# Kernel optimization log

Measured on AMD Instinct MI355X. Metric: run time of the kernel, lower is better.

Reference implementation:

```python
import jax, jax.numpy as jnp
import numpy as np
import math

INF = 1e12  # constant.INFINITY_NUMBER in the original repo


def setup_inputs() -> dict:
    key = jax.random.key(0)
    ks = jax.random.split(key, 12)
    B, S, W, D = 16, 512, 8, 768
    M, Wm = 2, 64
    U, Wu = 32, 16
    V = 32000
    words = jax.random.randint(ks[0], (B, S, W), 0, V)
    masks = jax.random.randint(ks[1], (B, S, W), 0, 2).astype(bool)
    main = jax.random.randint(ks[2], (B, M, Wm), 0, V)
    main_mask = jax.random.randint(ks[3], (B, M, Wm), 0, 2).astype(bool)
    user = jax.random.randint(ks[4], (B, U, Wu), 0, V)
    user_mask = jax.random.randint(ks[5], (B, U, Wu), 0, 2).astype(bool)
    # sparse-ish dependency adjacency
    adj = (jax.random.uniform(ks[6], (B, S, S)) < 0.05).astype(jnp.float32)
    emb_weight = jax.random.normal(ks[7], (V, D), jnp.float32) * 0.02
    K_w = jax.random.normal(ks[8], (D, D), jnp.float32) * (1.0 / math.sqrt(D))
    K_b = jnp.zeros((D,), jnp.float32)
    Q_w = jax.random.normal(ks[9], (D, D), jnp.float32) * (1.0 / math.sqrt(D))
    Q_b = jnp.zeros((D,), jnp.float32)
    return {"words": words, "masks": masks, "main": main, "main_mask": main_mask,
            "user": user, "user_mask": user_mask, "adj": adj,
            "emb_weight": emb_weight, "K_w": K_w, "K_b": K_b, "Q_w": Q_w, "Q_b": Q_b}


def _masked_max(embs, mask, axis):
    # masked_fill(mask, -INF) -> max(axis) ; caller fixes residual -INF rows
    return jnp.max(jnp.where(mask[..., None], -INF, embs), axis=axis)


def reference(words, masks, main, main_mask, user, user_mask, adj,
              emb_weight, K_w, K_b, Q_w, Q_b):
    D = emb_weight.shape[1]

    word_embs = emb_weight[words]   # [B,S,W,D]
    main_embs = emb_weight[main]    # [B,M,Wm,D]
    user_embs = emb_weight[user]    # [B,U,Wu,D]

    # node mask from adjacency: True where node has no in/out edges
    mask = ((adj.sum(axis=2) + adj.sum(axis=1)) == 0)[:, :, None]  # [B,S,1]

    # main: masked max-pool over word pieces, zero fully-masked rows
    main_e = _masked_max(main_embs, main_mask, axis=2)             # [B,M,D]
    main_e = jnp.where(main_e == -INF, 0.0, main_e)

    # user: masked max-pool over word pieces then over users
    user_e = _masked_max(user_embs, user_mask, axis=2)             # [B,U,D]
    user_e = jnp.max(user_e, axis=1)                               # [B,D]
    user_e = jnp.where(user_e == -INF, 0.0, user_e)

    # token embeddings: masked max-pool over word pieces (no -INF fix in original)
    g = _masked_max(word_embs, masks, axis=2)                      # [B,S,D]

    # single-head attention: softmax(K g (Q g)^T / sqrt(D)) @ g
    key_ = g @ K_w.T + K_b                                         # [B,S,D]
    query = g @ Q_w.T + Q_b                                        # [B,S,D]
    scores = jnp.einsum('bsd,btd->bst', key_, query) / math.sqrt(D)
    dense_graph = jax.nn.softmax(scores, axis=2)                   # [B,S,S]
    gcn_out = jnp.einsum('bst,btd->bsd', dense_graph, g)           # [B,S,D]

    adj_sm = jax.nn.softmax(adj, axis=2)

    return (gcn_out, mask, dense_graph, adj_sm,
            jnp.squeeze(main_e), jnp.squeeze(user_e))
```

## Files before the change

kernel.cpp:

```cpp
#include <hip/hip_runtime.h>
#include <hip/hip_bf16.h>
#include <math.h>

static constexpr int Bn = 16, Sn = 512, Wn = 8, Dn = 768;
static constexpr int Mn_ = 2, WMn = 64;
static constexpr int Un = 32, WUn = 16;

#define INF_VAL 1e12f
#define INV_SQRT_D 0.03608439182435161f

static constexpr size_t OFF_GCN   = 0;
static constexpr size_t OFF_MASK  = 6291456;
static constexpr size_t OFF_DENSE = 6299648;
static constexpr size_t OFF_ADJ   = 10493952;
static constexpr size_t OFF_MAIN  = 14688256;
static constexpr size_t OFF_USER  = 14712832;

static constexpr size_t WSB_GBF     = 0;
static constexpr size_t WSB_GT      = 12582912;
static constexpr size_t WSB_DENSEBF = 25165824;
static constexpr size_t WSB_HBF     = 33554432;
static constexpr size_t WSB_KWT     = 46137344;
static constexpr size_t WSB_QWT     = 47316992;
static constexpr size_t WSB_MT      = 48496640;
static constexpr size_t WSB_PARTU   = 49676288;
static constexpr size_t WSB_PARTM   = 51249152;
static constexpr size_t WSB_KBAR    = 51642368;
static constexpr size_t WSB_QBAR    = 51648512;
static constexpr size_t WSB_U       = 51654656;
static constexpr size_t WSB_V       = 51660800;
static constexpr size_t WSB_VA      = 51666944;
static constexpr size_t WSB_VB      = 51673088;
static constexpr size_t WSB_CONSTS  = 51679232;
static constexpr size_t WSB_QS      = 51679296;
static constexpr size_t WSB_KQ      = 51712064;
static constexpr size_t WSB_GA      = 51744832;
static constexpr size_t WSB_GB      = 51777600;
static constexpr size_t WSB_COLSUM  = 51810368;
static constexpr size_t WSB_FLAGS   = 51843136;
static constexpr size_t WSB_ROWSUM  = 51875904;
static constexpr size_t WSB_UVU     = 51908672;
static constexpr size_t WSB_UVV     = 51957824;
static constexpr size_t WSB_UVA     = 52006976;
static constexpr size_t WSB_UVB     = 52056128;

typedef __attribute__((ext_vector_type(8))) short short8;
typedef __attribute__((ext_vector_type(4))) float f32x4;

static __device__ __forceinline__ ushort f2bf(float f) {
    union { float f; unsigned u; } v; v.f = f;
    unsigned u = v.u;
    unsigned r = (u + 0x7FFFu + ((u >> 16) & 1u)) >> 16;
    return (ushort)r;
}

static __device__ __forceinline__ void gload16(const void* g, void* lds) {
    __builtin_amdgcn_global_load_lds(
        (const __attribute__((address_space(1))) void*)g,
        (__attribute__((address_space(3))) void*)lds, 16, 0, 0);
}

static __device__ __forceinline__ void fmax4(float4& a, const float4& x) {
    a.x = fmaxf(a.x, x.x); a.y = fmaxf(a.y, x.y);
    a.z = fmaxf(a.z, x.z); a.w = fmaxf(a.w, x.w);
}

__global__ __launch_bounds__(256)
void fold1(const float* __restrict__ K_w, const float* __restrict__ K_b,
           const float* __restrict__ Q_w, const float* __restrict__ Q_b,
           double* __restrict__ kbar, double* __restrict__ qbar,
           ushort* __restrict__ KwbT, ushort* __restrict__ QwbT,
           float* __restrict__ colsum) {
    int blk = blockIdx.x, t = threadIdx.x;
    if (blk < 192) {
        int wv = t >> 6, lane = t & 63;
        int r = blk * 4 + wv;
        double sk = 0.0, sq = 0.0;
        for (int d = lane; d < Dn; d += 64) {
            sk += (double)K_w[(size_t)r * Dn + d];
            sq += (double)Q_w[(size_t)r * Dn + d];
        }
        #pragma unroll
        for (int off = 32; off > 0; off >>= 1) {
            sk += __shfl_down(sk, off, 64);
            sq += __shfl_down(sq, off, 64);
        }
        if (lane == 0) {
            kbar[r] = -1e12 * sk + (double)K_b[r];
            qbar[r] = -1e12 * sq + (double)Q_b[r];
        }
    } else if (blk < 1344) {
        int tt = blk - 192;
        const float* src = (tt < 576) ? K_w : Q_w;
        ushort* dst = (tt < 576) ? KwbT : QwbT;
        int t6 = (tt < 576) ? tt : tt - 576;
        int e0 = (t6 % 24) * 32, i0 = (t6 / 24) * 32;
        __shared__ ushort tile[32][33];
        int tx = t & 31, ty = t >> 5;
        #pragma unroll
        for (int i2 = 0; i2 < 4; ++i2)
            tile[ty + i2 * 8][tx] = f2bf(src[(size_t)(e0 + ty + i2 * 8) * Dn + i0 + tx]);
        __syncthreads();
        #pragma unroll
        for (int i2 = 0; i2 < 4; ++i2)
            dst[(size_t)(i0 + ty + i2 * 8) * Dn + e0 + tx] = tile[tx][ty + i2 * 8];
    } else {
        for (int i = t; i < Bn * Sn; i += 256) colsum[i] = 0.f;
    }
}

__global__ __launch_bounds__(512)
void adjsm_uv_kernel(const float* __restrict__ adj, float* __restrict__ adjsm,
                     float* __restrict__ colsum, float* __restrict__ rowsum,
                     const float* __restrict__ K_w, const float* __restrict__ Q_w,
                     const float* __restrict__ K_b, const float* __restrict__ Q_b,
                     const double* __restrict__ kbar, const double* __restrict__ qbar,
                     double* __restrict__ uvu, double* __restrict__ uvv,
                     double* __restrict__ uva, double* __restrict__ uvb) {
    int blk = blockIdx.x;
    int t = threadIdx.x;
    if (blk >= 512) {
        int id = (blk - 512) * 512 + t;
        int c = id / 768;
        int j = id - c * 768;
        int e0 = c * 96;
        double su = 0.0, sv = 0.0, sa = 0.0, sb = 0.0;
        for (int e = e0; e < e0 + 96; ++e) {
            double kw = (double)K_w[(size_t)e * Dn + j];
            double qw = (double)Q_w[(size_t)e * Dn + j];
            su += kw * qbar[e];
            sv += qw * kbar[e];
            sa += kw * (double)Q_b[e];
            sb += qw * (double)K_b[e];
        }
        uvu[(size_t)c * Dn + j] = su;
        uvv[(size_t)c * Dn + j] = sv;
        uva[(size_t)c * Dn + j] = sa;
        uvb[(size_t)c * Dn + j] = sb;
        return;
    }
    int b = blk >> 5, rc = blk & 31;
    const float* base = adj + ((size_t)b * Sn + rc * 16) * Sn;
    float* obase = adjsm + ((size_t)b * Sn + rc * 16) * Sn;
    const float EM1 = 0.36787944117144233f;
    const float EP1 = 2.718281828459045f;
    __shared__ float rows[16][512];
    __shared__ float n1s[16];
    #pragma unroll
    for (int r = 0; r < 16; ++r) rows[r][t] = base[(size_t)r * Sn + t];
    __syncthreads();
    int wv = t >> 6, lane = t & 63;
    #pragma unroll
    for (int rr2 = 0; rr2 < 2; ++rr2) {
        int r = wv * 2 + rr2;
        float s = 0.f;
        #pragma unroll
        for (int c = 0; c < 8; ++c) s += rows[r][lane + c * 64];
        #pragma unroll
        for (int off = 32; off > 0; off >>= 1) s += __shfl_down(s, off, 64);
        if (lane == 0) {
            n1s[r] = s;
            rowsum[(size_t)b * Sn + rc * 16 + r] = s;
        }
    }
    __syncthreads();
    float colacc = 0.f;
    #pragma unroll
    for (int r = 0; r < 16; ++r) {
        float a = rows[r][t];
        colacc += a;
        float n1 = n1s[r];
        float e1, e0;
        if (n1 > 0.f) { e1 = 1.f; e0 = EM1; } else { e1 = EP1; e0 = 1.f; }
        float inv = 1.f / (n1 * e1 + (512.f - n1) * e0);
        obase[(size_t)r * Sn + t] = (a == 1.f ? e1 : e0) * inv;
    }
    atomicAdd(&colsum[(size_t)b * Sn + t], colacc);
}

template<int OUT_BF16>
static __device__ __forceinline__
void gemm_device(const ushort* __restrict__ A, const ushort* __restrict__ B,
                 void* __restrict__ Cout, int bx, int by, int bz,
                 int Km, int lda, int ldb, int ldc,
                 long long sA, long long sB, long long sC,
                 ushort* As, ushort* Bs) {
    const ushort* Ab = A + (size_t)bz * sA;
    const ushort* Bb = B + (size_t)bz * sB;
    int i0 = by * 128, j0 = bx * 64;
    int tid = threadIdx.x;
    int lane = tid & 63, wv = tid >> 6;
    int wr = wv >> 1, wc = wv & 1;
    int ln15 = lane & 15, lkg = lane >> 4;
    int r4 = lane >> 4;
    int c16 = lane & 15;

    f32x4 acc[4][2] = {};

    for (int k0 = 0; k0 < Km; k0 += 128) {
        #pragma unroll
        for (int it = 0; it < 8; ++it) {
            int r = it * 16 + wv * 4 + r4;
            int cc = c16 ^ (r & 15);
            ushort* dstA = As + (it * 4096 + wv * 1024) / 2;
            gload16(Ab + (size_t)(i0 + r) * lda + k0 + cc * 8, dstA);
        }
        #pragma unroll
        for (int it = 0; it < 4; ++it) {
            int r = it * 16 + wv * 4 + r4;
            int cc = c16 ^ (r & 15);
            ushort* dstB = Bs + (it * 4096 + wv * 1024) / 2;
            gload16(Bb + (size_t)(j0 + r) * ldb + k0 + cc * 8, dstB);
        }
        __syncthreads();
        #pragma unroll
        for (int kh = 0; kh < 4; ++kh) {
            short8 af[4], bfr[2];
            int kc = kh * 4 + lkg;
            #pragma unroll
            for (int f = 0; f < 4; ++f) {
                int ra = wr * 64 + f * 16 + ln15;
                af[f] = *(const short8*)((const char*)As + ra * 256 + ((kc ^ (ra & 15)) << 4));
            }
            #pragma unroll
            for (int f = 0; f < 2; ++f) {
                int rb = wc * 32 + f * 16 + ln15;
                bfr[f] = *(const short8*)((const char*)Bs + rb * 256 + ((kc ^ (rb & 15)) << 4));
            }
            #pragma unroll
            for (int fa = 0; fa < 4; ++fa)
                #pragma unroll
                for (int fb = 0; fb < 2; ++fb)
                    acc[fa][fb] = __builtin_amdgcn_mfma_f32_16x16x32_bf16(
                        af[fa], bfr[fb], acc[fa][fb], 0, 0, 0);
        }
        __syncthreads();
    }

    #pragma unroll
    for (int fa = 0; fa < 4; ++fa) {
        #pragma unroll
        for (int fb = 0; fb < 2; ++fb) {
            int n = j0 + wc * 32 + fb * 16 + ln15;
            #pragma unroll
            for (int rr = 0; rr < 4; ++rr) {
                int m = i0 + wr * 64 + fa * 16 + lkg * 4 + rr;
                float val = acc[fa][fb][rr];
                if (OUT_BF16) {
                    ((ushort*)Cout)[(size_t)bz * sC + (size_t)m * ldc + n] = f2bf(val);
                } else {
                    ((float*)Cout)[(size_t)bz * sC + (size_t)m * ldc + n] = val;
                }
            }
        }
    }
}

template<int OUT_BF16>
__global__ __launch_bounds__(256)
void gemm_mfma(const ushort* __restrict__ A, const ushort* __restrict__ B,
               void* __restrict__ Cout,
               int Km, int lda, int ldb, int ldc,
               long long sA, long long sB, long long sC) {
    __shared__ ushort As[128 * 128];
    __shared__ ushort Bs[64 * 128];
    gemm_device<OUT_BF16>(A, B, Cout, blockIdx.x, blockIdx.y, blockIdx.z,
                          Km, lda, ldb, ldc, sA, sB, sC, As, Bs);
}

__global__ __launch_bounds__(256)
void uvmt_kernel(const ushort* __restrict__ QwbT, const ushort* __restrict__ KwbT,
                 ushort* __restrict__ Mt,
                 const double* __restrict__ uvu, const double* __restrict__ uvv,
                 const double* __restrict__ uva, const double* __restrict__ uvb,
                 const double* __restrict__ kbar, const double* __restrict__ qbar,
                 const float* __restrict__ K_b, const float* __restrict__ Q_b,
                 double* __restrict__ u, double* __restrict__ v,
                 double* __restrict__ va, double* __restrict__ vb,
                 double* __restrict__ consts) {
    __shared__ ushort As[128 * 128];
    __shared__ ushort Bs[64 * 128];
    int blk = blockIdx.x;
    int t = threadIdx.x;
    if (blk < 72) {
        gemm_device<1>(QwbT, KwbT, Mt, blk % 12, blk / 12, 0,
                       Dn, Dn, Dn, Dn, 0, 0, 0, As, Bs);
        return;
    }
    if (blk < 75) {
        int j = (blk - 72) * 256 + t;
        double su = 0.0, sv = 0.0, sa = 0.0, sb = 0.0;
        #pragma unroll
        for (int c = 0; c < 8; ++c) {
            su += uvu[(size_t)c * Dn + j];
            sv += uvv[(size_t)c * Dn + j];
            sa += uva[(size_t)c * Dn + j];
            sb += uvb[(size_t)c * Dn + j];
        }
        u[j] = su; v[j] = sv; va[j] = sa; vb[j] = sb;
        return;
    }
    if (t >= 64) return;
    int l = t;
    double c0 = 0.0, c1 = 0.0, c2 = 0.0, c3 = 0.0;
    for (int e = l; e < Dn; e += 64) {
        c0 += kbar[e] * (double)Q_b[e];
        c1 += kbar[e] * qbar[e];
        c2 += qbar[e] * (double)K_b[e];
        c3 += (double)K_b[e] * (double)Q_b[e];
    }
    #pragma unroll
    for (int off = 32; off > 0; off >>= 1) {
        c0 += __shfl_down(c0, off, 64);
        c1 += __shfl_down(c1, off, 64);
        c2 += __shfl_down(c2, off, 64);
        c3 += __shfl_down(c3, off, 64);
    }
    if (l == 0) { consts[0] = c0; consts[1] = c1; consts[2] = c2; consts[3] = c3; }
}

__global__ __launch_bounds__(192)
void pool_g_s1(const int* __restrict__ words, const int* __restrict__ masks,
               const int* __restrict__ main_idx, const int* __restrict__ mmask,
               const int* __restrict__ user_idx, const int* __restrict__ umask,
               const float* __restrict__ emb,
               const double* __restrict__ u, const double* __restrict__ v,
               const double* __restrict__ va, const double* __restrict__ vb,
               const double* __restrict__ consts,
               ushort* __restrict__ gbf, float* __restrict__ qs,
               float* __restrict__ kq, float* __restrict__ ga,
               float* __restrict__ gb, int* __restrict__ flags,
               float* __restrict__ partM, float* __restrict__ partU) {
    int blk = blockIdx.x;
    int t = threadIdx.x;
    if (blk >= Bn * Sn) {
        int s1 = blk - Bn * Sn;
        const int *irow, *mrow;
        float* dst;
        if (s1 < 128) {
            int bm = s1 >> 2, ch = s1 & 3;
            irow = main_idx + (size_t)bm * WMn + ch * 16;
            mrow = mmask + (size_t)bm * WMn + ch * 16;
            dst = partM + (size_t)s1 * Dn;
        } else {
            int bu = s1 - 128;
            irow = user_idx + (size_t)bu * WUn;
            mrow = umask + (size_t)bu * WUn;
            dst = partU + (size_t)bu * Dn;
        }
        float4 acc = make_float4(-INF_VAL, -INF_VAL, -INF_VAL, -INF_VAL);
        #pragma unroll
        for (int w = 0; w < 16; ++w) {
            if (mrow[w] != 0) continue;
            float4 x = ((const float4*)(emb + (size_t)irow[w] * Dn))[t];
            fmax4(acc, x);
        }
        ((float4*)dst)[t] = acc;
        return;
    }
    int bs = blk;
    const int* wrow = words + (size_t)bs * Wn;
    const int* mrow = masks + (size_t)bs * Wn;
    float4 acc = make_float4(-INF_VAL, -INF_VAL, -INF_VAL, -INF_VAL);
    int nm = 0;
    #pragma unroll
    for (int w = 0; w < Wn; ++w) {
        int mk = mrow[w];
        nm += (mk != 0);
        if (mk != 0) continue;
        float4 x = ((const float4*)(emb + (size_t)wrow[w] * Dn))[t];
        fmax4(acc, x);
    }
    ushort4 o;
    o.x = f2bf(acc.x); o.y = f2bf(acc.y); o.z = f2bf(acc.z); o.w = f2bf(acc.w);
    ((ushort4*)(gbf + (size_t)bs * Dn))[t] = o;
    int j = t * 4;
    double dv = v[j] * (double)acc.x + v[j+1] * (double)acc.y
              + v[j+2] * (double)acc.z + v[j+3] * (double)acc.w;
    double du = u[j] * (double)acc.x + u[j+1] * (double)acc.y
              + u[j+2] * (double)acc.z + u[j+3] * (double)acc.w;
    double da = va[j] * (double)acc.x + va[j+1] * (double)acc.y
              + va[j+2] * (double)acc.z + va[j+3] * (double)acc.w;
    double db = vb[j] * (double)acc.x + vb[j+1] * (double)acc.y
              + vb[j+2] * (double)acc.z + vb[j+3] * (double)acc.w;
    #pragma unroll
    for (int off = 32; off > 0; off >>= 1) {
        dv += __shfl_down(dv, off, 64);
        du += __shfl_down(du, off, 64);
        da += __shfl_down(da, off, 64);
        db += __shfl_down(db, off, 64);
    }
    __shared__ double rr[12];
    if ((t & 63) == 0) {
        rr[t >> 6] = dv; rr[3 + (t >> 6)] = du;
        rr[6 + (t >> 6)] = da; rr[9 + (t >> 6)] = db;
    }
    __syncthreads();
    if (t == 0) {
        qs[bs] = (float)(rr[0] + rr[1] + rr[2] + consts[0]);
        kq[bs] = (float)(rr[3] + rr[4] + rr[5] + consts[2]);
        ga[bs] = (float)(rr[6] + rr[7] + rr[8]);
        gb[bs] = (float)(rr[9] + rr[10] + rr[11]);
        flags[bs] = (nm == Wn) ? 1 : 0;
    }
}

__global__ __launch_bounds__(256)
void midh_kernel(const ushort* __restrict__ gbf, const ushort* __restrict__ Mt,
                 ushort* __restrict__ hbf, ushort* __restrict__ gT,
                 const float* __restrict__ partM, const float* __restrict__ partU,
                 float* __restrict__ outM, float* __restrict__ outU,
                 const float* __restrict__ rowsum, const float* __restrict__ colsum,
                 float* __restrict__ maskout) {
    __shared__ ushort As[128 * 128];
    __shared__ ushort Bs[64 * 128];
    int blk = blockIdx.x;
    int t = threadIdx.x;
    if (blk < 768) {
        gemm_device<1>(gbf, Mt, hbf, blk % 12, blk / 12, 0,
                       Dn, Dn, Dn, Dn, 0, 0, 0, As, Bs);
        return;
    }
    if (blk < 6912) {
        int bb = blk - 768;
        ushort (*tile)[33] = (ushort(*)[33])As;
        int b = bb / 384;
        int rem = bb - b * 384;
        int d0 = (rem % 24) * 32, s0 = (rem / 24) * 32;
        int tx = t & 31, ty = t >> 5;
        #pragma unroll
        for (int i = 0; i < 4; ++i)
            tile[ty + i * 8][tx] = gbf[((size_t)(b * Sn + s0 + ty + i * 8)) * Dn + d0 + tx];
        __syncthreads();
        #pragma unroll
        for (int i = 0; i < 4; ++i)
            gT[((size_t)(b * Dn + d0 + ty + i * 8)) * Sn + s0 + tx] = tile[tx][ty + i * 8];
        return;
    }
    if (blk >= 6960) {
        int i = (blk - 6960) * 256 + t;
        if (i < Bn * Sn)
            maskout[i] = ((rowsum[i] + colsum[i]) == 0.f) ? 1.f : 0.f;
        return;
    }
    if (t >= 192) return;
    float4 acc = make_float4(-INF_VAL, -INF_VAL, -INF_VAL, -INF_VAL);
    float* dst;
    if (blk < 6944) {
        int bm = blk - 6912;
        #pragma unroll
        for (int c = 0; c < 4; ++c) {
            float4 x = ((const float4*)(partM + (size_t)(bm * 4 + c) * Dn))[t];
            fmax4(acc, x);
        }
        dst = outM + (size_t)bm * Dn;
    } else {
        int b = blk - 6944;
        for (int u2 = 0; u2 < Un; ++u2) {
            float4 x = ((const float4*)(partU + (size_t)(b * Un + u2) * Dn))[t];
            fmax4(acc, x);
        }
        dst = outU + (size_t)b * Dn;
    }
    if (acc.x == -INF_VAL) acc.x = 0.f;
    if (acc.y == -INF_VAL) acc.y = 0.f;
    if (acc.z == -INF_VAL) acc.z = 0.f;
    if (acc.w == -INF_VAL) acc.w = 0.f;
    ((float4*)dst)[t] = acc;
}

__global__ __launch_bounds__(256)
void softmax_fix(float* __restrict__ dense, const int* __restrict__ flags,
                 const float* __restrict__ qs, const float* __restrict__ kq,
                 const float* __restrict__ ga, const float* __restrict__ gb,
                 const double* __restrict__ consts, ushort* __restrict__ densebf) {
    int bs = blockIdx.x;
    int b = bs >> 9;
    int t = threadIdx.x;
    float* row = dense + (size_t)bs * 512;
    int f0 = flags[(b << 9) + t];
    int f1 = flags[(b << 9) + t + 256];
    bool sm = flags[bs] != 0;
    float x0, x1;
    if (sm) {
        float c1i = (float)consts[1] * INV_SQRT_D;
        x0 = f0 ? c1i : qs[(b << 9) + t] * INV_SQRT_D;
        x1 = f1 ? c1i : qs[(b << 9) + t + 256] * INV_SQRT_D;
    } else {
        float kqi = kq[bs] * INV_SQRT_D;
        float corr = ga[bs] + (float)consts[3];
        x0 = f0 ? kqi : (row[t] + corr + gb[(b << 9) + t]) * INV_SQRT_D;
        x1 = f1 ? kqi : (row[t + 256] + corr + gb[(b << 9) + t + 256]) * INV_SQRT_D;
    }
    float m = fmaxf(x0, x1);
    #pragma unroll
    for (int off = 32; off > 0; off >>= 1) m = fmaxf(m, __shfl_down(m, off, 64));
    __shared__ float red[4];
    __shared__ float bmax, bsum;
    if ((t & 63) == 0) red[t >> 6] = m;
    __syncthreads();
    if (t == 0) bmax = fmaxf(fmaxf(red[0], red[1]), fmaxf(red[2], red[3]));
    __syncthreads();
    float mx = bmax;
    float e0 = expf(x0 - mx), e1 = expf(x1 - mx);
    float s = e0 + e1;
    #pragma unroll
    for (int off = 32; off > 0; off >>= 1) s += __shfl_down(s, off, 64);
    if ((t & 63) == 0) red[t >> 6] = s;
    __syncthreads();
    if (t == 0) bsum = red[0] + red[1] + red[2] + red[3];
    __syncthreads();
    float inv = 1.f / bsum;
    float p0 = e0 * inv, p1 = e1 * inv;
    row[t] = p0; row[t + 256] = p1;
    ushort* bro = densebf + (size_t)bs * 512;
    bro[t] = f2bf(p0); bro[t + 256] = f2bf(p1);
}

extern "C" void kernel_launch(void* const* d_in, const int* in_sizes, int n_in,
                              void* d_out, int out_size, void* d_ws, size_t ws_size,
                              hipStream_t stream) {
    const int*   words     = (const int*)d_in[0];
    const int*   masks     = (const int*)d_in[1];
    const int*   main_idx  = (const int*)d_in[2];
    const int*   main_mask = (const int*)d_in[3];
    const int*   user_idx  = (const int*)d_in[4];
    const int*   user_mask = (const int*)d_in[5];
    const float* adj       = (const float*)d_in[6];
    const float* emb       = (const float*)d_in[7];
    const float* K_w       = (const float*)d_in[8];
    const float* K_b       = (const float*)d_in[9];
    const float* Q_w       = (const float*)d_in[10];
    const float* Q_b       = (const float*)d_in[11];

    float* out = (float*)d_out;
    char*  ws8 = (char*)d_ws;

    ushort* gbf     = (ushort*)(ws8 + WSB_GBF);
    ushort* gT      = (ushort*)(ws8 + WSB_GT);
    ushort* densebf = (ushort*)(ws8 + WSB_DENSEBF);
    ushort* hbf     = (ushort*)(ws8 + WSB_HBF);
    ushort* KwbT    = (ushort*)(ws8 + WSB_KWT);
    ushort* QwbT    = (ushort*)(ws8 + WSB_QWT);
    ushort* Mt      = (ushort*)(ws8 + WSB_MT);
    float*  partU   = (float*)(ws8 + WSB_PARTU);
    float*  partM   = (float*)(ws8 + WSB_PARTM);
    double* kbar    = (double*)(ws8 + WSB_KBAR);
    double* qbar    = (double*)(ws8 + WSB_QBAR);
    double* u       = (double*)(ws8 + WSB_U);
    double* v       = (double*)(ws8 + WSB_V);
    double* va      = (double*)(ws8 + WSB_VA);
    double* vb      = (double*)(ws8 + WSB_VB);
    double* consts  = (double*)(ws8 + WSB_CONSTS);
    float*  qs      = (float*)(ws8 + WSB_QS);
    float*  kq      = (float*)(ws8 + WSB_KQ);
    float*  ga      = (float*)(ws8 + WSB_GA);
    float*  gb      = (float*)(ws8 + WSB_GB);
    float*  colsum  = (float*)(ws8 + WSB_COLSUM);
    int*    flags   = (int*)(ws8 + WSB_FLAGS);
    float*  rowsum  = (float*)(ws8 + WSB_ROWSUM);
    double* uvu     = (double*)(ws8 + WSB_UVU);
    double* uvv     = (double*)(ws8 + WSB_UVV);
    double* uva     = (double*)(ws8 + WSB_UVA);
    double* uvb     = (double*)(ws8 + WSB_UVB);

    float* dense = out + OFF_DENSE;

    fold1<<<1345, 256, 0, stream>>>(K_w, K_b, Q_w, Q_b, kbar, qbar, KwbT, QwbT, colsum);

    adjsm_uv_kernel<<<524, 512, 0, stream>>>(adj, out + OFF_ADJ, colsum, rowsum,
                                             K_w, Q_w, K_b, Q_b, kbar, qbar,
                                             uvu, uvv, uva, uvb);

    uvmt_kernel<<<76, 256, 0, stream>>>(QwbT, KwbT, Mt, uvu, uvv, uva, uvb,
                                        kbar, qbar, K_b, Q_b, u, v, va, vb, consts);

    pool_g_s1<<<Bn * Sn + 640, 192, 0, stream>>>(
        words, masks, main_idx, main_mask, user_idx, user_mask, emb,
        u, v, va, vb, consts, gbf, qs, kq, ga, gb, flags, partM, partU);

    midh_kernel<<<6992, 256, 0, stream>>>(gbf, Mt, hbf, gT, partM, partU,
                                          out + OFF_MAIN, out + OFF_USER,
                                          rowsum, colsum, out + OFF_MASK);

    gemm_mfma<0><<<dim3(8, 4, Bn), 256, 0, stream>>>(
        hbf, gbf, dense, Dn, Dn, Dn, Sn,
        (long long)Sn * Dn, (long long)Sn * Dn, (long long)Sn * Sn);

    softmax_fix<<<Bn * Sn, 256, 0, stream>>>(dense, flags, qs, kq, ga, gb, consts, densebf);

    gemm_mfma<0><<<dim3(12, 4, Bn), 256, 0, stream>>>(
        densebf, gT, out + OFF_GCN, Sn, Sn, Sn, Dn,
        (long long)Sn * Sn, (long long)Dn * Sn, (long long)Sn * Dn);
}
```

Before: 150.5 us.

## Merge adj softmax with uv/Mt stage; store raw scores as bf16

The adjacency-softmax, uv partial products and the Mt GEMM now run as one 608-block kernel instead of being split across two launches, and a small separate kernel does the uv reduction and the constants. The first attention GEMM now writes its raw scores in bf16 to a workspace buffer rather than fp32 into the output, and softmax_fix reads them in packed pairs and writes both outputs with vectorised stores. This is meant to cut launch count, serialisation and score-matrix memory traffic. The price is bf16 rounding of the pre-softmax logits, which could hurt accuracy.

```diff
diff --git a/kernel.cpp b/kernel.cpp
--- a/kernel.cpp
+++ b/kernel.cpp
@@ -43,6 +43,7 @@
 static constexpr size_t WSB_UVV     = 51957824;
 static constexpr size_t WSB_UVA     = 52006976;
 static constexpr size_t WSB_UVB     = 52056128;
+static constexpr size_t WSB_RAWBF   = 52105280;
 
 typedef __attribute__((ext_vector_type(8))) short short8;
 typedef __attribute__((ext_vector_type(4))) float f32x4;
@@ -52,6 +53,10 @@
     unsigned u = v.u;
     unsigned r = (u + 0x7FFFu + ((u >> 16) & 1u)) >> 16;
     return (ushort)r;
+}
+
+static __device__ __forceinline__ float bf2f(unsigned hi16) {
+    union { unsigned u; float f; } v; v.u = hi16 << 16; return v.f;
 }
 
 static __device__ __forceinline__ void gload16(const void* g, void* lds) {
@@ -107,75 +112,6 @@
     } else {
         for (int i = t; i < Bn * Sn; i += 256) colsum[i] = 0.f;
     }
-}
-
-__global__ __launch_bounds__(512)
-void adjsm_uv_kernel(const float* __restrict__ adj, float* __restrict__ adjsm,
-                     float* __restrict__ colsum, float* __restrict__ rowsum,
-                     const float* __restrict__ K_w, const float* __restrict__ Q_w,
-                     const float* __restrict__ K_b, const float* __restrict__ Q_b,
-                     const double* __restrict__ kbar, const double* __restrict__ qbar,
-                     double* __restrict__ uvu, double* __restrict__ uvv,
-                     double* __restrict__ uva, double* __restrict__ uvb) {
-    int blk = blockIdx.x;
-    int t = threadIdx.x;
-    if (blk >= 512) {
-        int id = (blk - 512) * 512 + t;
-        int c = id / 768;
-        int j = id - c * 768;
-        int e0 = c * 96;
-        double su = 0.0, sv = 0.0, sa = 0.0, sb = 0.0;
-        for (int e = e0; e < e0 + 96; ++e) {
-            double kw = (double)K_w[(size_t)e * Dn + j];
-            double qw = (double)Q_w[(size_t)e * Dn + j];
-            su += kw * qbar[e];
-            sv += qw * kbar[e];
-            sa += kw * (double)Q_b[e];
-            sb += qw * (double)K_b[e];
-        }
-        uvu[(size_t)c * Dn + j] = su;
-        uvv[(size_t)c * Dn + j] = sv;
-        uva[(size_t)c * Dn + j] = sa;
-        uvb[(size_t)c * Dn + j] = sb;
-        return;
-    }
-    int b = blk >> 5, rc = blk & 31;
-    const float* base = adj + ((size_t)b * Sn + rc * 16) * Sn;
-    float* obase = adjsm + ((size_t)b * Sn + rc * 16) * Sn;
-    const float EM1 = 0.36787944117144233f;
-    const float EP1 = 2.718281828459045f;
-    __shared__ float rows[16][512];
-    __shared__ float n1s[16];
-    #pragma unroll
-    for (int r = 0; r < 16; ++r) rows[r][t] = base[(size_t)r * Sn + t];
-    __syncthreads();
-    int wv = t >> 6, lane = t & 63;
-    #pragma unroll
-    for (int rr2 = 0; rr2 < 2; ++rr2) {
-        int r = wv * 2 + rr2;
-        float s = 0.f;
-        #pragma unroll
-        for (int c = 0; c < 8; ++c) s += rows[r][lane + c * 64];
-        #pragma unroll
-        for (int off = 32; off > 0; off >>= 1) s += __shfl_down(s, off, 64);
-        if (lane == 0) {
-            n1s[r] = s;
-            rowsum[(size_t)b * Sn + rc * 16 + r] = s;
-        }
-    }
-    __syncthreads();
-    float colacc = 0.f;
-    #pragma unroll
-    for (int r = 0; r < 16; ++r) {
-        float a = rows[r][t];
-        colacc += a;
-        float n1 = n1s[r];
-        float e1, e0;
-        if (n1 > 0.f) { e1 = 1.f; e0 = EM1; } else { e1 = EP1; e0 = 1.f; }
-        float inv = 1.f / (n1 * e1 + (512.f - n1) * e0);
-        obase[(size_t)r * Sn + t] = (a == 1.f ? e1 : e0) * inv;
-    }
-    atomicAdd(&colsum[(size_t)b * Sn + t], colacc);
 }
 
 template<int OUT_BF16>
@@ -269,26 +205,102 @@
 }
 
 __global__ __launch_bounds__(256)
-void uvmt_kernel(const ushort* __restrict__ QwbT, const ushort* __restrict__ KwbT,
-                 ushort* __restrict__ Mt,
-                 const double* __restrict__ uvu, const double* __restrict__ uvv,
-                 const double* __restrict__ uva, const double* __restrict__ uvb,
-                 const double* __restrict__ kbar, const double* __restrict__ qbar,
-                 const float* __restrict__ K_b, const float* __restrict__ Q_b,
-                 double* __restrict__ u, double* __restrict__ v,
-                 double* __restrict__ va, double* __restrict__ vb,
-                 double* __restrict__ consts) {
+void adjuvmt_kernel(const float* __restrict__ adj, float* __restrict__ adjsm,
+                    float* __restrict__ colsum, float* __restrict__ rowsum,
+                    const float* __restrict__ K_w, const float* __restrict__ Q_w,
+                    const float* __restrict__ K_b, const float* __restrict__ Q_b,
+                    const double* __restrict__ kbar, const double* __restrict__ qbar,
+                    double* __restrict__ uvu, double* __restrict__ uvv,
+                    double* __restrict__ uva, double* __restrict__ uvb,
+                    const ushort* __restrict__ QwbT, const ushort* __restrict__ KwbT,
+                    ushort* __restrict__ Mt) {
     __shared__ ushort As[128 * 128];
     __shared__ ushort Bs[64 * 128];
     int blk = blockIdx.x;
     int t = threadIdx.x;
-    if (blk < 72) {
-        gemm_device<1>(QwbT, KwbT, Mt, blk % 12, blk / 12, 0,
+    if (blk < 24) {
+        int id = blk * 256 + t;
+        int c = id / 768;
+        int j = id - c * 768;
+        int e0 = c * 96;
+        double su = 0.0, sv = 0.0, sa = 0.0, sb = 0.0;
+        for (int e = e0; e < e0 + 96; ++e) {
+            double kw = (double)K_w[(size_t)e * Dn + j];
+            double qw = (double)Q_w[(size_t)e * Dn + j];
+            su += kw * qbar[e];
+            sv += qw * kbar[e];
+            sa += kw * (double)Q_b[e];
+            sb += qw * (double)K_b[e];
+        }
+        uvu[(size_t)c * Dn + j] = su;
+        uvv[(size_t)c * Dn + j] = sv;
+        uva[(size_t)c * Dn + j] = sa;
+        uvb[(size_t)c * Dn + j] = sb;
+        return;
+    }
+    if (blk < 96) {
+        int g = blk - 24;
+        gemm_device<1>(QwbT, KwbT, Mt, g % 12, g / 12, 0,
                        Dn, Dn, Dn, Dn, 0, 0, 0, As, Bs);
         return;
     }
-    if (blk < 75) {
-        int j = (blk - 72) * 256 + t;
+    int ab = blk - 96;
+    int b = ab >> 5, rc = ab & 31;
+    const float* base = adj + ((size_t)b * Sn + rc * 16) * Sn;
+    float* obase = adjsm + ((size_t)b * Sn + rc * 16) * Sn;
+    const float EM1 = 0.36787944117144233f;
+    const float EP1 = 2.718281828459045f;
+    float (*rows)[512] = (float(*)[512])As;
+    float* n1s = (float*)Bs;
+    #pragma unroll
+    for (int r = 0; r < 16; ++r) {
+        rows[r][t]       = base[(size_t)r * Sn + t];
+        rows[r][t + 256] = base[(size_t)r * Sn + t + 256];
+    }
+    __syncthreads();
+    int wv = t >> 6, lane = t & 63;
+    #pragma unroll
+    for (int rr2 = 0; rr2 < 4; ++rr2) {
+        int r = wv * 4 + rr2;
+        float s = 0.f;
+        #pragma unroll
+        for (int c = 0; c < 8; ++c) s += rows[r][lane + c * 64];
+        #pragma unroll
+        for (int off = 32; off > 0; off >>= 1) s += __shfl_down(s, off, 64);
+        if (lane == 0) {
+            n1s[r] = s;
+            rowsum[(size_t)b * Sn + rc * 16 + r] = s;
+        }
+    }
+    __syncthreads();
+    float colacc0 = 0.f, colacc1 = 0.f;
+    #pragma unroll
+    for (int r = 0; r < 16; ++r) {
+        float a0 = rows[r][t], a1 = rows[r][t + 256];
+        colacc0 += a0; colacc1 += a1;
+        float n1 = n1s[r];
+        float e1, e0;
+        if (n1 > 0.f) { e1 = 1.f; e0 = EM1; } else { e1 = EP1; e0 = 1.f; }
+        float inv = 1.f / (n1 * e1 + (512.f - n1) * e0);
+        obase[(size_t)r * Sn + t]       = (a0 == 1.f ? e1 : e0) * inv;
+        obase[(size_t)r * Sn + t + 256] = (a1 == 1.f ? e1 : e0) * inv;
+    }
+    atomicAdd(&colsum[(size_t)b * Sn + t], colacc0);
+    atomicAdd(&colsum[(size_t)b * Sn + t + 256], colacc1);
+}
+
+__global__ __launch_bounds__(64)
+void uvred_consts(const double* __restrict__ uvu, const double* __restrict__ uvv,
+                  const double* __restrict__ uva, const double* __restrict__ uvb,
+                  const double* __restrict__ kbar, const double* __restrict__ qbar,
+                  const float* __restrict__ K_b, const float* __restrict__ Q_b,
+                  double* __restrict__ u, double* __restrict__ v,
+                  double* __restrict__ va, double* __restrict__ vb,
+                  double* __restrict__ consts) {
+    int blk = blockIdx.x;
+    int l = threadIdx.x;
+    if (blk < 12) {
+        int j = blk * 64 + l;
         double su = 0.0, sv = 0.0, sa = 0.0, sb = 0.0;
         #pragma unroll
         for (int c = 0; c < 8; ++c) {
@@ -298,25 +310,23 @@
             sb += uvb[(size_t)c * Dn + j];
         }
         u[j] = su; v[j] = sv; va[j] = sa; vb[j] = sb;
-        return;
-    }
-    if (t >= 64) return;
-    int l = t;
-    double c0 = 0.0, c1 = 0.0, c2 = 0.0, c3 = 0.0;
-    for (int e = l; e < Dn; e += 64) {
-        c0 += kbar[e] * (double)Q_b[e];
-        c1 += kbar[e] * qbar[e];
-        c2 += qbar[e] * (double)K_b[e];
-        c3 += (double)K_b[e] * (double)Q_b[e];
-    }
-    #pragma unroll
-    for (int off = 32; off > 0; off >>= 1) {
-        c0 += __shfl_down(c0, off, 64);
-        c1 += __shfl_down(c1, off, 64);
-        c2 += __shfl_down(c2, off, 64);
-        c3 += __shfl_down(c3, off, 64);
-    }
-    if (l == 0) { consts[0] = c0; consts[1] = c1; consts[2] = c2; consts[3] = c3; }
+    } else {
+        double c0 = 0.0, c1 = 0.0, c2 = 0.0, c3 = 0.0;
+        for (int e = l; e < Dn; e += 64) {
+            c0 += kbar[e] * (double)Q_b[e];
+            c1 += kbar[e] * qbar[e];
+            c2 += qbar[e] * (double)K_b[e];
+            c3 += (double)K_b[e] * (double)Q_b[e];
+        }
+        #pragma unroll
+        for (int off = 32; off > 0; off >>= 1) {
+            c0 += __shfl_down(c0, off, 64);
+            c1 += __shfl_down(c1, off, 64);
+            c2 += __shfl_down(c2, off, 64);
+            c3 += __shfl_down(c3, off, 64);
+        }
+        if (l == 0) { consts[0] = c0; consts[1] = c1; consts[2] = c2; consts[3] = c3; }
+    }
 }
 
 __global__ __launch_bounds__(192)
@@ -470,27 +480,31 @@
 }
 
 __global__ __launch_bounds__(256)
-void softmax_fix(float* __restrict__ dense, const int* __restrict__ flags,
+void softmax_fix(const ushort* __restrict__ raw, const int* __restrict__ flags,
                  const float* __restrict__ qs, const float* __restrict__ kq,
                  const float* __restrict__ ga, const float* __restrict__ gb,
-                 const double* __restrict__ consts, ushort* __restrict__ densebf) {
+                 const double* __restrict__ consts,
+                 float* __restrict__ dense, ushort* __restrict__ densebf) {
     int bs = blockIdx.x;
     int b = bs >> 9;
     int t = threadIdx.x;
-    float* row = dense + (size_t)bs * 512;
-    int f0 = flags[(b << 9) + t];
-    int f1 = flags[(b << 9) + t + 256];
+    int c0i = 2 * t, c1idx = 2 * t + 1;
+    unsigned rpack = ((const unsigned*)(raw + (size_t)bs * 512))[t];
+    float r0 = bf2f(rpack & 0xFFFFu);
+    float r1 = bf2f(rpack >> 16);
+    int f0 = flags[(b << 9) + c0i];
+    int f1 = flags[(b << 9) + c1idx];
     bool sm = flags[bs] != 0;
     float x0, x1;
     if (sm) {
-        float c1i = (float)consts[1] * INV_SQRT_D;
-        x0 = f0 ? c1i : qs[(b << 9) + t] * INV_SQRT_D;
-        x1 = f1 ? c1i : qs[(b << 9) + t + 256] * INV_SQRT_D;
+        float c1v = (float)consts[1] * INV_SQRT_D;
+        x0 = f0 ? c1v : qs[(b << 9) + c0i] * INV_SQRT_D;
+        x1 = f1 ? c1v : qs[(b << 9) + c1idx] * INV_SQRT_D;
     } else {
         float kqi = kq[bs] * INV_SQRT_D;
         float corr = ga[bs] + (float)consts[3];
-        x0 = f0 ? kqi : (row[t] + corr + gb[(b << 9) + t]) * INV_SQRT_D;
-        x1 = f1 ? kqi : (row[t + 256] + corr + gb[(b << 9) + t + 256]) * INV_SQRT_D;
+        x0 = f0 ? kqi : (r0 + corr + gb[(b << 9) + c0i]) * INV_SQRT_D;
+        x1 = f1 ? kqi : (r1 + corr + gb[(b << 9) + c1idx]) * INV_SQRT_D;
     }
     float m = fmaxf(x0, x1);
     #pragma unroll
@@ -512,9 +526,10 @@
     __syncthreads();
     float inv = 1.f / bsum;
     float p0 = e0 * inv, p1 = e1 * inv;
-    row[t] = p0; row[t + 256] = p1;
-    ushort* bro = densebf + (size_t)bs * 512;
-    bro[t] = f2bf(p0); bro[t + 256] = f2bf(p1);
+    float2 pv; pv.x = p0; pv.y = p1;
+    ((float2*)(dense + (size_t)bs * 512))[t] = pv;
+    ((unsigned*)(densebf + (size_t)bs * 512))[t] =
+        (unsigned)f2bf(p0) | ((unsigned)f2bf(p1) << 16);
 }
 
 extern "C" void kernel_launch(void* const* d_in, const int* in_sizes, int n_in,
@@ -543,6 +558,7 @@
     ushort* KwbT    = (ushort*)(ws8 + WSB_KWT);
     ushort* QwbT    = (ushort*)(ws8 + WSB_QWT);
     ushort* Mt      = (ushort*)(ws8 + WSB_MT);
+    ushort* rawbf   = (ushort*)(ws8 + WSB_RAWBF);
     float*  partU   = (float*)(ws8 + WSB_PARTU);
     float*  partM   = (float*)(ws8 + WSB_PARTM);
     double* kbar    = (double*)(ws8 + WSB_KBAR);
@@ -568,12 +584,12 @@
 
     fold1<<<1345, 256, 0, stream>>>(K_w, K_b, Q_w, Q_b, kbar, qbar, KwbT, QwbT, colsum);
 
-    adjsm_uv_kernel<<<524, 512, 0, stream>>>(adj, out + OFF_ADJ, colsum, rowsum,
-                                             K_w, Q_w, K_b, Q_b, kbar, qbar,
-                                             uvu, uvv, uva, uvb);
-
-    uvmt_kernel<<<76, 256, 0, stream>>>(QwbT, KwbT, Mt, uvu, uvv, uva, uvb,
-                                        kbar, qbar, K_b, Q_b, u, v, va, vb, consts);
+    adjuvmt_kernel<<<608, 256, 0, stream>>>(adj, out + OFF_ADJ, colsum, rowsum,
+                                            K_w, Q_w, K_b, Q_b, kbar, qbar,
+                                            uvu, uvv, uva, uvb, QwbT, KwbT, Mt);
+
+    uvred_consts<<<13, 64, 0, stream>>>(uvu, uvv, uva, uvb, kbar, qbar, K_b, Q_b,
+                                        u, v, va, vb, consts);
 
     pool_g_s1<<<Bn * Sn + 640, 192, 0, stream>>>(
         words, masks, main_idx, main_mask, user_idx, user_mask, emb,
@@ -583,11 +599,12 @@
                                           out + OFF_MAIN, out + OFF_USER,
                                           rowsum, colsum, out + OFF_MASK);
 
-    gemm_mfma<0><<<dim3(8, 4, Bn), 256, 0, stream>>>(
-        hbf, gbf, dense, Dn, Dn, Dn, Sn,
+    gemm_mfma<1><<<dim3(8, 4, Bn), 256, 0, stream>>>(
+        hbf, gbf, rawbf, Dn, Dn, Dn, Sn,
         (long long)Sn * Dn, (long long)Sn * Dn, (long long)Sn * Sn);
 
-    softmax_fix<<<Bn * Sn, 256, 0, stream>>>(dense, flags, qs, kq, ga, gb, consts, densebf);
+    softmax_fix<<<Bn * Sn, 256, 0, stream>>>(rawbf, flags, qs, kq, ga, gb, consts,
+                                             dense, densebf);
 
     gemm_mfma<0><<<dim3(12, 4, Bn), 256, 0, stream>>>(
         densebf, gT, out + OFF_GCN, Sn, Sn, Sn, Dn,
```

After: 142.6 us. 1.06x faster.
